# Kernel optimization log

Measured on AMD Instinct MI355X. Metric: run time of the kernel, lower is better.

The kernel has to match this reference:

```python
import jax, jax.numpy as jnp
import numpy as np

D = 512
HEAD_NUMB = 8

def setup_inputs() -> dict:
    key = jax.random.key(0)
    k1, k2, k3 = jax.random.split(key, 3)
    x = jax.random.normal(k1, (4, 4096, D), dtype=jnp.float32)
    # nn.Linear(D, 3D): weight [3D, D], bias [3D]
    W_qkv = jax.random.normal(k2, (3 * D, D), dtype=jnp.float32) / np.sqrt(D)
    b_qkv = jax.random.normal(k3, (3 * D,), dtype=jnp.float32) * 0.01
    return {"x": x, "W_qkv": W_qkv, "b_qkv": b_qkv}

def reference(x, W_qkv, b_qkv):
    # fused QKV projection: x @ W^T + b  -> [B, N, 3D]
    qkv = jnp.einsum('bnd,ed->bne', x, W_qkv) + b_qkv
    q = qkv[:, :, :D]
    k = qkv[:, :, D:2 * D]
    v = qkv[:, :, 2 * D:]
    scaling = (D / HEAD_NUMB) ** (-0.5)
    # single-head attention over full D (faithful to the original module)
    scores = jnp.einsum('bqd,bkd->bqk', q, k) * scaling  # [B, N, N]
    attn = jax.nn.softmax(scores, axis=2)
    return jnp.einsum('bqk,bkd->bqd', attn, v)
```

## Files before the change

### kernel.cpp

```cpp
#include <hip/hip_runtime.h>
#include <hip/hip_bf16.h>

#define D_DIM 512
#define NSEQ  4096
#define BATCH 4
#define SCALE 0.125f

typedef __attribute__((ext_vector_type(8)))  short short8;
typedef __attribute__((ext_vector_type(16))) float floatx16;

__device__ __forceinline__ unsigned short f2bf(float f) {
    __hip_bfloat16 h = __float2bfloat16(f);
    return *reinterpret_cast<unsigned short*>(&h);
}

__device__ __forceinline__ floatx16 mfma_bf16(short8 a, short8 b, floatx16 c) {
    return __builtin_amdgcn_mfma_f32_32x32x16_bf16(a, b, c, 0, 0, 0);
}

#define K1_STRIDE 40

__global__ __launch_bounds__(256, 2) void qkv_gemm(
    const float* __restrict__ x, const float* __restrict__ W,
    const float* __restrict__ bias,
    unsigned short* __restrict__ qs, unsigned short* __restrict__ kk,
    unsigned short* __restrict__ vT)
{
    __shared__ __align__(16) unsigned short Xs[128 * K1_STRIDE];
    __shared__ __align__(16) unsigned short Ws[128 * K1_STRIDE];

    const int t = threadIdx.x;
    const int lane = t & 63, w = t >> 6;
    const int l31 = lane & 31, lh = lane >> 5;
    const int wm = w >> 1, we = w & 1;
    const int m0 = blockIdx.x * 128;
    const int n0 = blockIdx.y * 128;

    floatx16 a00, a01, a10, a11;
#pragma unroll
    for (int r = 0; r < 16; r++) { a00[r] = 0.f; a01[r] = 0.f; a10[r] = 0.f; a11[r] = 0.f; }

    for (int kc = 0; kc < 16; kc++) {
        const int k0 = kc * 32;
        __syncthreads();
#pragma unroll
        for (int p = 0; p < 4; p++) {
            int id = t + p * 256;
            int row = id >> 3, kq = id & 7;
            float4 xv = *(const float4*)(x + (size_t)(m0 + row) * D_DIM + k0 + 4 * kq);
            ushort4 hx; hx.x = f2bf(xv.x); hx.y = f2bf(xv.y); hx.z = f2bf(xv.z); hx.w = f2bf(xv.w);
            *(ushort4*)&Xs[row * K1_STRIDE + 4 * kq] = hx;
            float4 wv = *(const float4*)(W + (size_t)(n0 + row) * D_DIM + k0 + 4 * kq);
            ushort4 hw; hw.x = f2bf(wv.x); hw.y = f2bf(wv.y); hw.z = f2bf(wv.z); hw.w = f2bf(wv.w);
            *(ushort4*)&Ws[row * K1_STRIDE + 4 * kq] = hw;
        }
        __syncthreads();
#pragma unroll
        for (int ks = 0; ks < 2; ks++) {
            const int co = ks * 16 + lh * 8;
            short8 fa0 = *(const short8*)&Xs[(wm * 64 + l31) * K1_STRIDE + co];
            short8 fa1 = *(const short8*)&Xs[(wm * 64 + 32 + l31) * K1_STRIDE + co];
            short8 fb0 = *(const short8*)&Ws[(we * 64 + l31) * K1_STRIDE + co];
            short8 fb1 = *(const short8*)&Ws[(we * 64 + 32 + l31) * K1_STRIDE + co];
            a00 = mfma_bf16(fa0, fb0, a00);
            a01 = mfma_bf16(fa0, fb1, a01);
            a10 = mfma_bf16(fa1, fb0, a10);
            a11 = mfma_bf16(fa1, fb1, a11);
        }
    }

#pragma unroll
    for (int jt = 0; jt < 2; jt++) {
        const int e = n0 + we * 64 + jt * 32 + l31;
        const float bv = bias[e];
#pragma unroll
        for (int it = 0; it < 2; it++) {
            const int mb = m0 + wm * 64 + it * 32;
            const floatx16& av = (it == 0) ? ((jt == 0) ? a00 : a01)
                                           : ((jt == 0) ? a10 : a11);
            if (e < 512) {
#pragma unroll
                for (int r = 0; r < 16; r++) {
                    int m = mb + (r & 3) + 8 * (r >> 2) + 4 * lh;
                    qs[(size_t)m * D_DIM + e] = f2bf((av[r] + bv) * SCALE);
                }
            } else if (e < 1024) {
#pragma unroll
                for (int r = 0; r < 16; r++) {
                    int m = mb + (r & 3) + 8 * (r >> 2) + 4 * lh;
                    kk[(size_t)m * D_DIM + (e - 512)] = f2bf(av[r] + bv);
                }
            } else {
                const int d = e - 1024;
#pragma unroll
                for (int q = 0; q < 4; q++) {
                    int mq = mb + 8 * q + 4 * lh;
                    int bb = mq >> 12; int tok = mq & 4095;
                    ushort4 hv;
                    hv.x = f2bf(av[4 * q + 0] + bv); hv.y = f2bf(av[4 * q + 1] + bv);
                    hv.z = f2bf(av[4 * q + 2] + bv); hv.w = f2bf(av[4 * q + 3] + bv);
                    *(ushort4*)&vT[((size_t)bb * 512 + d) * 4096 + tok] = hv;
                }
            }
        }
    }
}

#define FA_BQ 64
#define FA_BK 256
#define FA_DC 128
#define QC_STR 136
#define KC_STR 136
#define P_STR  264
#define VT_STR 72

__global__ __launch_bounds__(512, 2) void flash_attn(
    const unsigned short* __restrict__ qs, const unsigned short* __restrict__ kk,
    const unsigned short* __restrict__ vT, float* __restrict__ out)
{
    __shared__ __align__(16) unsigned char smem[123392];
    unsigned short* Qc = (unsigned short*)(smem);
    unsigned short* Kc = (unsigned short*)(smem + 17408);
    unsigned short* Vt = (unsigned short*)(smem);
    unsigned short* P  = (unsigned short*)(smem + 87040);
    float* pmax    = (float*)(smem + 120832);
    float* psum    = (float*)(smem + 121856);
    float* alpha_s = (float*)(smem + 122880);
    float* l_s     = (float*)(smem + 123136);

    const int t = threadIdx.x;
    const int lane = t & 63, w = t >> 6;
    const int l31 = lane & 31, lh = lane >> 5;
    const int wi = w & 1, wjj = w >> 1;
    const int b  = blockIdx.y;
    const int q0 = blockIdx.x * FA_BQ;
    const size_t qbase = ((size_t)b * NSEQ + q0) * D_DIM;
    const size_t kbase = (size_t)b * NSEQ * D_DIM;
    const size_t vbase = (size_t)b * D_DIM * NSEQ;

    const int i_my = wi * 32 + l31;

    floatx16 o00, o01, o10, o11;
#pragma unroll
    for (int r = 0; r < 16; r++) { o00[r] = 0.f; o01[r] = 0.f; o10[r] = 0.f; o11[r] = 0.f; }
    float m_st = -__builtin_inff(), l_st = 0.f;

    for (int kt = 0; kt < NSEQ; kt += FA_BK) {
        floatx16 s0, s1;
#pragma unroll
        for (int r = 0; r < 16; r++) { s0[r] = 0.f; s1[r] = 0.f; }

        for (int dc = 0; dc < D_DIM; dc += FA_DC) {
            __syncthreads();
#pragma unroll
            for (int p = 0; p < 2; p++) {
                int id = t + p * 512;
                int row = id >> 4, c8 = id & 15;
                uint4 v = *(const uint4*)(qs + qbase + (size_t)row * D_DIM + dc + c8 * 8);
                *(uint4*)&Qc[row * QC_STR + c8 * 8] = v;
            }
#pragma unroll
            for (int p = 0; p < 8; p++) {
                int id = t + p * 512;
                int row = id >> 4, c8 = id & 15;
                uint4 v = *(const uint4*)(kk + kbase + (size_t)(kt + row) * D_DIM + dc + c8 * 8);
                *(uint4*)&Kc[row * KC_STR + c8 * 8] = v;
            }
            __syncthreads();
            const unsigned short* kr0 = &Kc[(wjj * 64 + l31) * KC_STR];
            const unsigned short* kr1 = kr0 + 32 * KC_STR;
            const unsigned short* qr  = &Qc[i_my * QC_STR];
#pragma unroll
            for (int ks = 0; ks < 8; ks++) {
                const int co = ks * 16 + lh * 8;
                short8 fa0 = *(const short8*)(kr0 + co);
                short8 fa1 = *(const short8*)(kr1 + co);
                short8 fb  = *(const short8*)(qr + co);
                s0 = mfma_bf16(fa0, fb, s0);
                s1 = mfma_bf16(fa1, fb, s1);
            }
        }

        float mx = -__builtin_inff();
#pragma unroll
        for (int r = 0; r < 16; r++) mx = fmaxf(mx, fmaxf(s0[r], s1[r]));
        mx = fmaxf(mx, __shfl_xor(mx, 32));
        if (lh == 0) pmax[i_my * 4 + wjj] = mx;
        __syncthreads();
        float4 pm = *(float4*)&pmax[i_my * 4];
        const float m_new = fmaxf(m_st, fmaxf(fmaxf(pm.x, pm.y), fmaxf(pm.z, pm.w)));
        const float alpha = __expf(m_st - m_new);
        m_st = m_new;

        float sum = 0.f;
        {
            const int prow = i_my * P_STR;
#pragma unroll
            for (int q = 0; q < 4; q++) {
                float p0 = __expf(s0[4*q+0] - m_new), p1 = __expf(s0[4*q+1] - m_new);
                float p2 = __expf(s0[4*q+2] - m_new), p3 = __expf(s0[4*q+3] - m_new);
                sum += (p0 + p1) + (p2 + p3);
                ushort4 h; h.x = f2bf(p0); h.y = f2bf(p1); h.z = f2bf(p2); h.w = f2bf(p3);
                *(ushort4*)&P[prow + (wjj*2+0)*32 + 8*q + 4*lh] = h;
            }
#pragma unroll
            for (int q = 0; q < 4; q++) {
                float p0 = __expf(s1[4*q+0] - m_new), p1 = __expf(s1[4*q+1] - m_new);
                float p2 = __expf(s1[4*q+2] - m_new), p3 = __expf(s1[4*q+3] - m_new);
                sum += (p0 + p1) + (p2 + p3);
                ushort4 h; h.x = f2bf(p0); h.y = f2bf(p1); h.z = f2bf(p2); h.w = f2bf(p3);
                *(ushort4*)&P[prow + (wjj*2+1)*32 + 8*q + 4*lh] = h;
            }
        }
        sum += __shfl_xor(sum, 32);
        if (lh == 0) psum[i_my * 4 + wjj] = sum;
        if (lh == 0 && wjj == 0) alpha_s[i_my] = alpha;
        __syncthreads();
        float4 ps = *(float4*)&psum[i_my * 4];
        l_st = l_st * alpha + ((ps.x + ps.y) + (ps.z + ps.w));

        float av[2][16];
        bool ch = false;
#pragma unroll
        for (int it = 0; it < 2; it++)
#pragma unroll
            for (int q = 0; q < 4; q++) {
                float4 a4 = *(float4*)&alpha_s[it * 32 + 8 * q + 4 * lh];
                av[it][4*q+0] = a4.x; av[it][4*q+1] = a4.y;
                av[it][4*q+2] = a4.z; av[it][4*q+3] = a4.w;
                ch = ch || (a4.x != 1.f) || (a4.y != 1.f) || (a4.z != 1.f) || (a4.w != 1.f);
            }
        if (__any(ch)) {
#pragma unroll
            for (int r = 0; r < 16; r++) {
                o00[r] *= av[0][r]; o01[r] *= av[0][r];
                o10[r] *= av[1][r]; o11[r] *= av[1][r];
            }
        }

        for (int jc = 0; jc < 4; jc++) {
            __syncthreads();
#pragma unroll
            for (int p = 0; p < 8; p++) {
                int id = t + p * 512;
                int d = id >> 3, c8 = id & 7;
                uint4 v = *(const uint4*)(vT + vbase + (size_t)d * NSEQ + kt + jc * 64 + c8 * 8);
                *(uint4*)&Vt[d * VT_STR + c8 * 8] = v;
            }
            __syncthreads();
            const unsigned short* pr0 = &P[l31 * P_STR + jc * 64];
            const unsigned short* pr1 = &P[(32 + l31) * P_STR + jc * 64];
            const unsigned short* vr0 = &Vt[(w * 64 + l31) * VT_STR];
            const unsigned short* vr1 = vr0 + 32 * VT_STR;
#pragma unroll
            for (int js = 0; js < 4; js++) {
                const int co = js * 16 + lh * 8;
                short8 pa0 = *(const short8*)(pr0 + co);
                short8 pa1 = *(const short8*)(pr1 + co);
                short8 vb0 = *(const short8*)(vr0 + co);
                short8 vb1 = *(const short8*)(vr1 + co);
                o00 = mfma_bf16(pa0, vb0, o00);
                o01 = mfma_bf16(pa0, vb1, o01);
                o10 = mfma_bf16(pa1, vb0, o10);
                o11 = mfma_bf16(pa1, vb1, o11);
            }
        }
    }

    if (lh == 0 && wjj == 0) l_s[i_my] = l_st;
    __syncthreads();
    float iv[2][16];
#pragma unroll
    for (int it = 0; it < 2; it++)
#pragma unroll
        for (int q = 0; q < 4; q++) {
            float4 l4 = *(float4*)&l_s[it * 32 + 8 * q + 4 * lh];
            iv[it][4*q+0] = 1.f / l4.x; iv[it][4*q+1] = 1.f / l4.y;
            iv[it][4*q+2] = 1.f / l4.z; iv[it][4*q+3] = 1.f / l4.w;
        }
#pragma unroll
    for (int it = 0; it < 2; it++) {
        const floatx16& oa = (it == 0) ? o00 : o10;
        const floatx16& ob = (it == 0) ? o01 : o11;
#pragma unroll
        for (int r = 0; r < 16; r++) {
            const int i = it * 32 + (r & 3) + 8 * (r >> 2) + 4 * lh;
            const size_t rowb = ((size_t)b * NSEQ + q0 + i) * D_DIM;
            out[rowb + w * 64 + l31]      = oa[r] * iv[it][r];
            out[rowb + w * 64 + 32 + l31] = ob[r] * iv[it][r];
        }
    }
}

extern "C" void kernel_launch(void* const* d_in, const int* in_sizes, int n_in,
                              void* d_out, int out_size, void* d_ws, size_t ws_size,
                              hipStream_t stream)
{
    (void)in_sizes; (void)n_in; (void)out_size; (void)ws_size;
    const float* x    = (const float*)d_in[0];
    const float* W    = (const float*)d_in[1];
    const float* bias = (const float*)d_in[2];
    float* out = (float*)d_out;

    unsigned short* qs = (unsigned short*)d_ws;
    unsigned short* kk = qs + (size_t)16384 * 512;
    unsigned short* vT = kk + (size_t)16384 * 512;

    qkv_gemm<<<dim3(128, 12), 256, 0, stream>>>(x, W, bias, qs, kk, vT);
    flash_attn<<<dim3(NSEQ / FA_BQ, BATCH), 512, 0, stream>>>(qs, kk, vT, out);
}
```

Before: 356.8 us.

## Pre-cast inputs to bf16 and load GEMM tiles via direct global-to-LDS with swizzle

Adds a separate kernel that converts x and W to bf16 once, so the QKV GEMM reads half the bytes and no longer repeats the conversion. Its tiles are then loaded with global_load_lds (16-byte direct-to-LDS transfers) into an XOR-swizzled layout, and the K chunk per iteration doubles to 64. The cost is an extra kernel launch plus a full write and re-read of the bf16 copies through workspace memory.

```diff
diff --git a/kernel.cpp b/kernel.cpp
--- a/kernel.cpp
+++ b/kernel.cpp
@@ -18,16 +18,37 @@
     return __builtin_amdgcn_mfma_f32_32x32x16_bf16(a, b, c, 0, 0, 0);
 }
 
-#define K1_STRIDE 40
+#define GLOAD16(g, l) __builtin_amdgcn_global_load_lds( \
+    (const __attribute__((address_space(1))) unsigned int*)(g), \
+    (__attribute__((address_space(3))) unsigned int*)(l), 16, 0, 0)
+
+__global__ __launch_bounds__(256) void cast_inputs(
+    const float* __restrict__ x, const float* __restrict__ W,
+    unsigned short* __restrict__ xb, unsigned short* __restrict__ Wb)
+{
+    const size_t NX = (size_t)BATCH * NSEQ * D_DIM;
+    size_t i = ((size_t)blockIdx.x * 256 + threadIdx.x) * 8;
+    const float* src; unsigned short* dst;
+    if (i < NX) { src = x + i; dst = xb + i; }
+    else        { src = W + (i - NX); dst = Wb + (i - NX); }
+    float4 v0 = *(const float4*)(src);
+    float4 v1 = *(const float4*)(src + 4);
+    short8 h;
+    h[0] = (short)f2bf(v0.x); h[1] = (short)f2bf(v0.y);
+    h[2] = (short)f2bf(v0.z); h[3] = (short)f2bf(v0.w);
+    h[4] = (short)f2bf(v1.x); h[5] = (short)f2bf(v1.y);
+    h[6] = (short)f2bf(v1.z); h[7] = (short)f2bf(v1.w);
+    *(short8*)dst = h;
+}
 
 __global__ __launch_bounds__(256, 2) void qkv_gemm(
-    const float* __restrict__ x, const float* __restrict__ W,
+    const unsigned short* __restrict__ xb, const unsigned short* __restrict__ Wb,
     const float* __restrict__ bias,
     unsigned short* __restrict__ qs, unsigned short* __restrict__ kk,
     unsigned short* __restrict__ vT)
 {
-    __shared__ __align__(16) unsigned short Xs[128 * K1_STRIDE];
-    __shared__ __align__(16) unsigned short Ws[128 * K1_STRIDE];
+    __shared__ __align__(16) unsigned short Xs[128 * 64];
+    __shared__ __align__(16) unsigned short Ws[128 * 64];
 
     const int t = threadIdx.x;
     const int lane = t & 63, w = t >> 6;
@@ -40,28 +61,35 @@
 #pragma unroll
     for (int r = 0; r < 16; r++) { a00[r] = 0.f; a01[r] = 0.f; a10[r] = 0.f; a11[r] = 0.f; }
 
-    for (int kc = 0; kc < 16; kc++) {
-        const int k0 = kc * 32;
+    int rowp[4], colp[4];
+#pragma unroll
+    for (int p = 0; p < 4; p++) {
+        int o = p * 4096 + t * 16;
+        int row = o >> 7;
+        int sl  = ((o >> 4) & 7) ^ (row & 7);
+        rowp[p] = row; colp[p] = sl * 8;
+    }
+
+    for (int kc = 0; kc < 8; kc++) {
+        const int k0 = kc * 64;
         __syncthreads();
 #pragma unroll
         for (int p = 0; p < 4; p++) {
-            int id = t + p * 256;
-            int row = id >> 3, kq = id & 7;
-            float4 xv = *(const float4*)(x + (size_t)(m0 + row) * D_DIM + k0 + 4 * kq);
-            ushort4 hx; hx.x = f2bf(xv.x); hx.y = f2bf(xv.y); hx.z = f2bf(xv.z); hx.w = f2bf(xv.w);
-            *(ushort4*)&Xs[row * K1_STRIDE + 4 * kq] = hx;
-            float4 wv = *(const float4*)(W + (size_t)(n0 + row) * D_DIM + k0 + 4 * kq);
-            ushort4 hw; hw.x = f2bf(wv.x); hw.y = f2bf(wv.y); hw.z = f2bf(wv.z); hw.w = f2bf(wv.w);
-            *(ushort4*)&Ws[row * K1_STRIDE + 4 * kq] = hw;
+            GLOAD16(xb + (size_t)(m0 + rowp[p]) * D_DIM + k0 + colp[p],
+                    (char*)Xs + p * 4096 + (t & ~63) * 16);
+            GLOAD16(Wb + (size_t)(n0 + rowp[p]) * D_DIM + k0 + colp[p],
+                    (char*)Ws + p * 4096 + (t & ~63) * 16);
         }
         __syncthreads();
-#pragma unroll
-        for (int ks = 0; ks < 2; ks++) {
-            const int co = ks * 16 + lh * 8;
-            short8 fa0 = *(const short8*)&Xs[(wm * 64 + l31) * K1_STRIDE + co];
-            short8 fa1 = *(const short8*)&Xs[(wm * 64 + 32 + l31) * K1_STRIDE + co];
-            short8 fb0 = *(const short8*)&Ws[(we * 64 + l31) * K1_STRIDE + co];
-            short8 fb1 = *(const short8*)&Ws[(we * 64 + 32 + l31) * K1_STRIDE + co];
+        const int sw = l31 & 7;
+#pragma unroll
+        for (int ks = 0; ks < 4; ks++) {
+            const int s = ks * 2 + lh;
+            const int cof = ((s ^ sw) * 8);
+            short8 fa0 = *(const short8*)&Xs[(wm * 64 +      l31) * 64 + cof];
+            short8 fa1 = *(const short8*)&Xs[(wm * 64 + 32 + l31) * 64 + cof];
+            short8 fb0 = *(const short8*)&Ws[(we * 64 +      l31) * 64 + cof];
+            short8 fb1 = *(const short8*)&Ws[(we * 64 + 32 + l31) * 64 + cof];
             a00 = mfma_bf16(fa0, fb0, a00);
             a01 = mfma_bf16(fa0, fb1, a01);
             a10 = mfma_bf16(fa1, fb0, a10);
@@ -305,7 +333,10 @@
     unsigned short* qs = (unsigned short*)d_ws;
     unsigned short* kk = qs + (size_t)16384 * 512;
     unsigned short* vT = kk + (size_t)16384 * 512;
-
-    qkv_gemm<<<dim3(128, 12), 256, 0, stream>>>(x, W, bias, qs, kk, vT);
+    unsigned short* xb = vT + (size_t)BATCH * D_DIM * NSEQ;
+    unsigned short* Wb = xb + (size_t)16384 * 512;
+
+    cast_inputs<<<dim3(4480), 256, 0, stream>>>(x, W, xb, Wb);
+    qkv_gemm<<<dim3(128, 12), 256, 0, stream>>>(xb, Wb, bias, qs, kk, vT);
     flash_attn<<<dim3(NSEQ / FA_BQ, BATCH), 512, 0, stream>>>(qs, kk, vT, out);
 }
```

Result: faster. 341.9 us (-4.2%).
